# Kernel optimization log

Hardware: AMD Instinct MI355X
Metric: run time of the kernel (lower is better)

## Reference

```python
import jax, jax.numpy as jnp
import numpy as np

B, S_IMG, S_TXT, D, H, HD = 1, 2048, 512, 3072, 24, 128
A_TOK, A_DIM = 4, 1024
S_TOT = S_IMG + S_TXT
EPS = 1e-6
SCALE = 1.0


def _heads(x):
    # [B, S, D] -> [B, H, S, HD]
    return x.reshape(B, -1, H, HD).transpose(0, 2, 1, 3)


def _rms(x, w):
    return x * jax.lax.rsqrt(jnp.mean(x * x, axis=-1, keepdims=True) + EPS) * w


def _rope(x, cos, sin):
    # diffusers apply_rotary_emb, use_real=True, use_real_unbind_dim=-1
    xr = x.reshape(*x.shape[:-1], HD // 2, 2)
    x1, x2 = xr[..., 0], xr[..., 1]
    x_rot = jnp.stack([-x2, x1], axis=-1).reshape(x.shape)
    return x * cos + x_rot * sin


def _sdpa(q, k, v):
    scores = jnp.einsum('bhqd,bhkd->bhqk', q, k) / np.sqrt(HD).astype(np.float32)
    return jnp.einsum('bhqk,bhkd->bhqd', jax.nn.softmax(scores, axis=-1), v)


def setup_inputs() -> dict:
    key = jax.random.key(0)
    ks = jax.random.split(key, 24)
    s = 0.02
    inp = {
        'hidden_states': jax.random.normal(ks[0], (B, S_IMG, D), jnp.float32),
        'encoder_hidden_states': jax.random.normal(ks[1], (B, S_TXT, D), jnp.float32),
        'adapter_embeds': jax.random.normal(ks[2], (B, A_TOK, A_DIM), jnp.float32),
        'freqs_cos': jnp.cos(jax.random.normal(ks[3], (S_TOT, HD), jnp.float32)),
        'freqs_sin': jnp.sin(jax.random.normal(ks[3], (S_TOT, HD), jnp.float32)),
        'Wq': jax.random.normal(ks[4], (D, D), jnp.float32) * s,
        'bq': jnp.zeros((D,), jnp.float32),
        'Wk': jax.random.normal(ks[5], (D, D), jnp.float32) * s,
        'bk': jnp.zeros((D,), jnp.float32),
        'Wv': jax.random.normal(ks[6], (D, D), jnp.float32) * s,
        'bv': jnp.zeros((D,), jnp.float32),
        'norm_q_w': jnp.ones((HD,), jnp.float32),
        'norm_k_w': jnp.ones((HD,), jnp.float32),
        'Wq_add': jax.random.normal(ks[7], (D, D), jnp.float32) * s,
        'bq_add': jnp.zeros((D,), jnp.float32),
        'Wk_add': jax.random.normal(ks[8], (D, D), jnp.float32) * s,
        'bk_add': jnp.zeros((D,), jnp.float32),
        'Wv_add': jax.random.normal(ks[9], (D, D), jnp.float32) * s,
        'bv_add': jnp.zeros((D,), jnp.float32),
        'norm_added_q_w': jnp.ones((HD,), jnp.float32),
        'norm_added_k_w': jnp.ones((HD,), jnp.float32),
        'Wo': jax.random.normal(ks[10], (D, D), jnp.float32) * s,
        'bo': jnp.zeros((D,), jnp.float32),
        'Wo_add': jax.random.normal(ks[11], (D, D), jnp.float32) * s,
        'bo_add': jnp.zeros((D,), jnp.float32),
        'Wk_adapt': jax.random.normal(ks[12], (A_DIM, D), jnp.float32) * s,
        'Wv_adapt': jax.random.normal(ks[13], (A_DIM, D), jnp.float32) * s,
        'block_scaler': jnp.ones((1,), jnp.float32),
    }
    return inp


def reference(hidden_states, encoder_hidden_states, adapter_embeds, freqs_cos, freqs_sin,
              Wq, bq, Wk, bk, Wv, bv, norm_q_w, norm_k_w,
              Wq_add, bq_add, Wk_add, bk_add, Wv_add, bv_add,
              norm_added_q_w, norm_added_k_w, Wo, bo, Wo_add, bo_add,
              Wk_adapt, Wv_adapt, block_scaler):
    # image-token Q/K/V + per-head RMSNorm
    q = _rms(_heads(hidden_states @ Wq + bq), norm_q_w)
    k = _rms(_heads(hidden_states @ Wk + bk), norm_k_w)
    v = _heads(hidden_states @ Wv + bv)
    # text-token Q/K/V + per-head RMSNorm
    eq = _rms(_heads(encoder_hidden_states @ Wq_add + bq_add), norm_added_q_w)
    ek = _rms(_heads(encoder_hidden_states @ Wk_add + bk_add), norm_added_k_w)
    ev = _heads(encoder_hidden_states @ Wv_add + bv_add)
    # joint sequence: [text, image]
    q = jnp.concatenate([eq, q], axis=2)
    k = jnp.concatenate([ek, k], axis=2)
    v = jnp.concatenate([ev, v], axis=2)
    # RoPE on full joint sequence
    q = _rope(q, freqs_cos, freqs_sin)
    k = _rope(k, freqs_cos, freqs_sin)
    # main joint attention
    hs = _sdpa(q, k, v)                                    # [B,H,S_TOT,HD]
    hs = hs.transpose(0, 2, 1, 3).reshape(B, S_TOT, D)
    # adapter cross-attention (vision-direct branch)
    vd_k = _heads(adapter_embeds @ Wk_adapt)               # [B,H,A_TOK,HD]
    vd_v = _heads(adapter_embeds @ Wv_adapt)
    vd = _sdpa(q, vd_k, vd_v)
    vd = vd.transpose(0, 2, 1, 3).reshape(B, S_TOT, D)
    hs = hs + SCALE * (vd * block_scaler)
    # split back and project
    enc_out = hs[:, :S_TXT] @ Wo_add + bo_add
    img_out = hs[:, S_TXT:] @ Wo + bo
    return img_out, enc_out
```

## Files before the change

kernel.cpp:

```cpp
#include <hip/hip_runtime.h>

typedef unsigned short u16;
typedef short s16x8 __attribute__((ext_vector_type(8)));
typedef float f32x4 __attribute__((ext_vector_type(4)));

#define S_TXTC 512
#define S_TOTC 2560
#define DM 3072
#define NH 24
#define HDM 128

__device__ __forceinline__ float b2f(u16 u){ unsigned int i = ((unsigned int)u)<<16; float f; __builtin_memcpy(&f,&i,4); return f; }
__device__ __forceinline__ u16 f2b(float f){ unsigned int i; __builtin_memcpy(&i,&f,4); unsigned int r = i + 0x7FFFu + ((i>>16)&1u); return (u16)(r>>16); }
__device__ __forceinline__ s16x8 pk8(float4 a, float4 b){
  s16x8 r;
  r[0]=(short)f2b(a.x); r[1]=(short)f2b(a.y); r[2]=(short)f2b(a.z); r[3]=(short)f2b(a.w);
  r[4]=(short)f2b(b.x); r[5]=(short)f2b(b.y); r[6]=(short)f2b(b.z); r[7]=(short)f2b(b.w);
  return r;
}
__device__ __forceinline__ void g2l16(const void* g, void* l){
  __builtin_amdgcn_global_load_lds((const __attribute__((address_space(1))) void*)g,
                                   (__attribute__((address_space(3))) void*)l, 16, 0, 0);
}

__global__ __launch_bounds__(256) void fillv(float* __restrict__ p, int n, float v){
  int i = blockIdx.x*256 + threadIdx.x;
  if (i < n) p[i] = v;
}

__global__ __launch_bounds__(256) void cast_bf(const float* __restrict__ src, u16* __restrict__ dst, int n8){
  int i = blockIdx.x*256 + threadIdx.x;
  if (i < n8){
    float4 a = *(const float4*)(src + (size_t)i*8);
    float4 b = *(const float4*)(src + (size_t)i*8 + 4);
    *(s16x8*)(dst + (size_t)i*8) = pk8(a,b);
  }
}

__global__ __launch_bounds__(256) void catbias(const float* __restrict__ b0, const float* __restrict__ b1,
                                               const float* __restrict__ b2, float* __restrict__ dst){
  int i = blockIdx.x*256 + threadIdx.x;
  if (i < 9216) dst[i] = (i<3072)? b0[i] : (i<6144? b1[i-3072] : b2[i-6144]);
}

__global__ __launch_bounds__(256) void ktrans(const float* __restrict__ W, u16* __restrict__ Wt){
  __shared__ __align__(16) u16 t[64*72];
  int nt = blockIdx.x*64, kt_ = blockIdx.y*64;
  int tid = threadIdx.x;
  #pragma unroll
  for (int i=0;i<2;i++){
    int q = tid + 256*i;
    int r = q>>3, c8 = (q&7)*8;
    float4 f0 = *(const float4*)(W + (size_t)(kt_+r)*DM + nt + c8);
    float4 f1 = *(const float4*)(W + (size_t)(kt_+r)*DM + nt + c8 + 4);
    *(s16x8*)&t[r*72 + c8] = pk8(f0,f1);
  }
  __syncthreads();
  #pragma unroll
  for (int i=0;i<2;i++){
    int q = tid + 256*i;
    int n = q>>3, k8 = (q&7)*8;
    s16x8 v;
    #pragma unroll
    for (int j=0;j<8;j++) v[j] = (short)t[(k8+j)*72 + n];
    *(s16x8*)(Wt + (size_t)(nt+n)*DM + kt_ + k8) = v;
  }
}

template<int OUT32>
__device__ __forceinline__ void gcore(u16* la, u16* lb,
    const u16* __restrict__ A, const u16* __restrict__ Bt,
    const float* __restrict__ bias, void* __restrict__ Cv,
    int ldc, int rb, int crb, int cb){
  const int K = DM;
  int tid = threadIdx.x, w = tid>>6, l = tid&63, g = l>>4, c16 = l&15;
  int wr = (w>>1)*64, wc = (w&1)*64;
  f32x4 acc[4][4] = {};
  const u16* aL = A  + (size_t)(rb + w*32 + (l>>2))*K + (l&3)*8;
  const u16* bL = Bt + (size_t)(cb + w*32 + (l>>2))*K + (l&3)*8;
  u16* laB = la + w*1024;
  u16* lbB = lb + w*1024;
  for (int ks=0; ks<K; ks+=32){
    g2l16(aL + ks,              laB);
    g2l16(aL + 16*(size_t)K + ks, laB + 512);
    g2l16(bL + ks,              lbB);
    g2l16(bL + 16*(size_t)K + ks, lbB + 512);
    __syncthreads();
    s16x8 af[4], bf[4];
    #pragma unroll
    for (int m=0;m<4;m++) af[m] = *(const s16x8*)&la[(wr + m*16 + c16)*32 + g*8];
    #pragma unroll
    for (int n=0;n<4;n++) bf[n] = *(const s16x8*)&lb[(wc + n*16 + c16)*32 + g*8];
    #pragma unroll
    for (int m=0;m<4;m++)
      #pragma unroll
      for (int n=0;n<4;n++)
        acc[m][n] = __builtin_amdgcn_mfma_f32_16x16x32_bf16(af[m], bf[n], acc[m][n], 0,0,0);
    __syncthreads();
  }
  #pragma unroll
  for (int n=0;n<4;n++){
    int col = cb + wc + n*16 + c16;
    float bv = bias[col];
    #pragma unroll
    for (int m=0;m<4;m++){
      int r0 = crb + wr + m*16 + g*4;
      #pragma unroll
      for (int r=0;r<4;r++){
        float oo = acc[m][n][r] + bv;
        if (OUT32) ((float*)Cv)[(size_t)(r0+r)*ldc + col] = oo;
        else       ((u16*)Cv)[(size_t)(r0+r)*ldc + col] = f2b(oo);
      }
    }
  }
}

__global__ __launch_bounds__(256) void qkv_gemm(const u16* __restrict__ A, const u16* __restrict__ Bt,
                                                const float* __restrict__ bias, u16* __restrict__ C){
  __shared__ __align__(16) u16 la[4096];
  __shared__ __align__(16) u16 lb[4096];
  gcore<0>(la, lb, A, Bt, bias, C, 3*DM, blockIdx.x*128, blockIdx.x*128, blockIdx.y*128);
}

__global__ __launch_bounds__(256) void out_gemm(const u16* __restrict__ hsb,
    const u16* __restrict__ woT, const u16* __restrict__ woaT,
    const float* __restrict__ bo, const float* __restrict__ boa, float* __restrict__ out){
  __shared__ __align__(16) u16 la[4096];
  __shared__ __align__(16) u16 lb[4096];
  int bx = blockIdx.x;
  bool txt = (bx < 4);
  int rb = bx*128;
  const u16* Bt = txt? woaT : woT;
  const float* bias = txt? boa : bo;
  float* dst = txt? out + (size_t)2048*DM : out;
  int crb = txt? rb : rb - 512;
  gcore<1>(la, lb, hsb, Bt, bias, dst, DM, rb, crb, blockIdx.y*128);
}

__global__ __launch_bounds__(256) void epi_qk(
    const u16* __restrict__ qkvI, const u16* __restrict__ qkvT,
    const float* __restrict__ nqw, const float* __restrict__ nkw,
    const float* __restrict__ naq, const float* __restrict__ nak,
    const float* __restrict__ fcos, const float* __restrict__ fsin,
    u16* __restrict__ qh, u16* __restrict__ kh){
  int wid = blockIdx.x*4 + (threadIdx.x>>6);
  int lane = threadIdx.x&63;
  int which = wid / (NH*S_TOTC);
  int rem = wid % (NH*S_TOTC);
  int h = rem / S_TOTC, tok = rem % S_TOTC;
  const u16* src = ((tok<S_TXTC)? qkvT + (size_t)tok*(3*DM) : qkvI + (size_t)(tok-S_TXTC)*(3*DM))
                   + which*DM + h*HDM;
  const float* nw = which? ((tok<S_TXTC)? nak : nkw) : ((tok<S_TXTC)? naq : nqw);
  int d = lane*2;
  unsigned int u = *(const unsigned int*)(src + d);
  float x0 = b2f((u16)(u&0xffffu)), x1 = b2f((u16)(u>>16));
  float ss = x0*x0 + x1*x1;
  #pragma unroll
  for (int m=1;m<64;m<<=1) ss += __shfl_xor(ss, m);
  float rr = rsqrtf(ss*(1.f/128.f) + 1e-6f);
  float y0 = x0*rr*nw[d];
  float y1 = x1*rr*nw[d+1];
  float2 cc = *(const float2*)(fcos + (size_t)tok*HDM + d);
  float2 sn = *(const float2*)(fsin + (size_t)tok*HDM + d);
  float o0 = y0*cc.x - y1*sn.x;
  float o1 = y1*cc.y + y0*sn.y;
  u16* dst = (which? kh : qh) + ((size_t)h*S_TOTC + tok)*HDM + d;
  *(unsigned int*)dst = (unsigned int)f2b(o0) | ((unsigned int)f2b(o1)<<16);
}

__global__ __launch_bounds__(256) void epi_v(const u16* __restrict__ qkvI, const u16* __restrict__ qkvT,
                                             u16* __restrict__ vt){
  __shared__ __align__(16) u16 t[64*136];
  int h = blockIdx.x % NH, tb = blockIdx.x / NH;
  int tok0 = tb*64, tid = threadIdx.x;
  #pragma unroll
  for (int i=0;i<4;i++){
    int q = tid + 256*i;
    int tr = q>>4, c8 = (q&15)*8;
    int tok = tok0 + tr;
    const u16* src = ((tok<S_TXTC)? qkvT + (size_t)tok*(3*DM) : qkvI + (size_t)(tok-S_TXTC)*(3*DM))
                     + 2*DM + h*HDM;
    *(s16x8*)&t[tr*136 + c8] = *(const s16x8*)(src + c8);
  }
  __syncthreads();
  #pragma unroll
  for (int i=0;i<4;i++){
    int q = tid + 256*i;
    int d = q>>3, j8 = (q&7)*8;
    s16x8 v;
    #pragma unroll
    for (int j=0;j<8;j++) v[j] = (short)t[(j8+j)*136 + d];
    *(s16x8*)(vt + ((size_t)h*HDM + d)*S_TOTC + tok0 + j8) = v;
  }
}

__global__ __launch_bounds__(256) void adapterk(const float* __restrict__ ad, const float* __restrict__ Wk,
        const float* __restrict__ Wv, u16* __restrict__ vdk, u16* __restrict__ vdv){
  int wid = blockIdx.x*4 + (threadIdx.x>>6);
  int lane = threadIdx.x&63;
  int tensor = wid / (4*DM);
  int rem = wid % (4*DM);
  int tok = rem / DM, col = rem % DM;
  const float* Wp = tensor? Wv : Wk;
  float s = 0.f;
  #pragma unroll
  for (int i=0;i<16;i++){
    int k = lane + 64*i;
    s += ad[tok*1024 + k] * Wp[(size_t)k*DM + col];
  }
  #pragma unroll
  for (int m=1;m<64;m<<=1) s += __shfl_xor(s, m);
  if (lane==0){
    int hh = col>>7, d = col&127;
    (tensor? vdv : vdk)[(hh*4+tok)*HDM + d] = f2b(s);
  }
}

__global__ __launch_bounds__(256) void attnk(const u16* __restrict__ qh, const u16* __restrict__ kh,
    const u16* __restrict__ vt, const u16* __restrict__ vdk, const u16* __restrict__ vdv,
    const float* __restrict__ bscale, u16* __restrict__ hs){
  __shared__ __align__(16) u16 kts[64*136];
  __shared__ __align__(16) u16 vts[128*72];
  __shared__ __align__(16) u16 pwb[64*72];
  __shared__ __align__(16) u16 kad[16*136];
  __shared__ __align__(16) u16 vad[128*40];
  int h = blockIdx.y, qb = blockIdx.x*64;
  int tid = threadIdx.x, w = tid>>6, l = tid&63, g = l>>4, c16 = l&15;
  for (int e=tid; e<2048; e+=256){ int key=e>>7, d=e&127; kad[key*136+d] = (key<4)? vdk[(h*4+key)*HDM+d] : (u16)0; }
  for (int e=tid; e<4096; e+=256){ int d=e>>5, key=e&31; vad[d*40+key]   = (key<4)? vdv[(h*4+key)*HDM+d] : (u16)0; }
  int qrow = qb + w*16 + c16;
  s16x8 qf[4];
  #pragma unroll
  for (int kc=0;kc<4;kc++) qf[kc] = *(const s16x8*)(qh + ((size_t)h*S_TOTC + qrow)*HDM + kc*32 + g*8);
  f32x4 acc[8];
  #pragma unroll
  for (int dt=0;dt<8;dt++) acc[dt] = f32x4{0.f,0.f,0.f,0.f};
  float m_[4] = {-3e38f,-3e38f,-3e38f,-3e38f};
  float l_[4] = {0.f,0.f,0.f,0.f};
  const float scl = 0.08838834764831845f;
  const u16* khB = kh + (size_t)h*S_TOTC*HDM;
  const u16* vtB = vt + (size_t)h*HDM*S_TOTC;

  auto LOADT = [&](s16x8* kr, s16x8* vr, int kb){
    #pragma unroll
    for (int i=0;i<4;i++){
      int idx = tid + 256*i;
      kr[i] = *(const s16x8*)(khB + (size_t)(kb + (idx>>4))*HDM + (idx&15)*8);
      vr[i] = *(const s16x8*)(vtB + (size_t)(idx>>3)*S_TOTC + kb + (idx&7)*8);
    }
  };
  auto STORET = [&](s16x8* kr, s16x8* vr){
    #pragma unroll
    for (int i=0;i<4;i++){
      int idx = tid + 256*i;
      *(s16x8*)&kts[(idx>>4)*136 + (idx&15)*8] = kr[i];
      *(s16x8*)&vts[(idx>>3)*72 + (idx&7)*8] = vr[i];
    }
  };
  auto COMPUTE = [&](){
    f32x4 s[4];
    #pragma unroll
    for (int su=0;su<4;su++) s[su] = f32x4{0.f,0.f,0.f,0.f};
    __builtin_amdgcn_s_setprio(1);
    #pragma unroll
    for (int su=0;su<4;su++)
      #pragma unroll
      for (int kc=0;kc<4;kc++){
        s16x8 kf = *(const s16x8*)&kts[(su*16+c16)*136 + (kc*4+g)*8];
        s[su] = __builtin_amdgcn_mfma_f32_16x16x32_bf16(qf[kc], kf, s[su], 0,0,0);
      }
    __builtin_amdgcn_s_setprio(0);
    float tm[4], corr[4], rs[4];
    #pragma unroll
    for (int r=0;r<4;r++){
      #pragma unroll
      for (int su=0;su<4;su++) s[su][r] *= scl;
      tm[r] = fmaxf(fmaxf(s[0][r],s[1][r]), fmaxf(s[2][r],s[3][r]));
    }
    #pragma unroll
    for (int m=1;m<16;m<<=1)
      #pragma unroll
      for (int r=0;r<4;r++) tm[r] = fmaxf(tm[r], __shfl_xor(tm[r], m));
    #pragma unroll
    for (int r=0;r<4;r++){
      float mn = fmaxf(m_[r], tm[r]);
      corr[r] = __expf(m_[r]-mn);
      m_[r] = mn;
      rs[r] = 0.f;
      #pragma unroll
      for (int su=0;su<4;su++){ s[su][r] = __expf(s[su][r]-mn); rs[r] += s[su][r]; }
    }
    #pragma unroll
    for (int m=1;m<16;m<<=1)
      #pragma unroll
      for (int r=0;r<4;r++) rs[r] += __shfl_xor(rs[r], m);
    #pragma unroll
    for (int r=0;r<4;r++) l_[r] = l_[r]*corr[r] + rs[r];
    #pragma unroll
    for (int dt=0;dt<8;dt++)
      #pragma unroll
      for (int r=0;r<4;r++) acc[dt][r] *= corr[r];
    #pragma unroll
    for (int su=0;su<4;su++)
      #pragma unroll
      for (int r=0;r<4;r++)
        pwb[(w*16 + g*4 + r)*72 + su*16 + c16] = f2b(s[su][r]);
    s16x8 pf0 = *(const s16x8*)&pwb[(w*16 + c16)*72 + g*8];
    s16x8 pf1 = *(const s16x8*)&pwb[(w*16 + c16)*72 + 32 + g*8];
    __builtin_amdgcn_s_setprio(1);
    #pragma unroll
    for (int dt=0;dt<8;dt++){
      s16x8 vf0 = *(const s16x8*)&vts[(dt*16 + c16)*72 + g*8];
      acc[dt] = __builtin_amdgcn_mfma_f32_16x16x32_bf16(pf0, vf0, acc[dt], 0,0,0);
      s16x8 vf1 = *(const s16x8*)&vts[(dt*16 + c16)*72 + 32 + g*8];
      acc[dt] = __builtin_amdgcn_mfma_f32_16x16x32_bf16(pf1, vf1, acc[dt], 0,0,0);
    }
    __builtin_amdgcn_s_setprio(0);
  };

  s16x8 ka[4], va[4], kb2[4], vb2[4];
  LOADT(ka, va, 0);
  for (int kb=0; kb<S_TOTC; kb+=128){
    STORET(ka, va);
    __syncthreads();
    LOADT(kb2, vb2, kb+64);
    COMPUTE();
    __syncthreads();
    STORET(kb2, vb2);
    __syncthreads();
    if (kb+128 < S_TOTC) LOADT(ka, va, kb+128);
    COMPUTE();
    __syncthreads();
  }

  f32x4 s2 = {0.f,0.f,0.f,0.f};
  #pragma unroll
  for (int kc=0;kc<4;kc++){
    s16x8 kf = *(const s16x8*)&kad[c16*136 + (kc*4+g)*8];
    s2 = __builtin_amdgcn_mfma_f32_16x16x32_bf16(qf[kc], kf, s2, 0,0,0);
  }
  bool valid = (c16 < 4);
  float m2[4], l2[4];
  #pragma unroll
  for (int r=0;r<4;r++){ s2[r]*=scl; m2[r] = valid? s2[r] : -3e38f; }
  #pragma unroll
  for (int m=1;m<16;m<<=1)
    #pragma unroll
    for (int r=0;r<4;r++) m2[r] = fmaxf(m2[r], __shfl_xor(m2[r], m));
  #pragma unroll
  for (int r=0;r<4;r++){ float p = valid? __expf(s2[r]-m2[r]) : 0.f; s2[r]=p; l2[r]=p; }
  #pragma unroll
  for (int m=1;m<16;m<<=1)
    #pragma unroll
    for (int r=0;r<4;r++) l2[r] += __shfl_xor(l2[r], m);
  #pragma unroll
  for (int r=0;r<4;r++){
    pwb[(w*16 + g*4 + r)*72 + c16]      = f2b(s2[r]);
    pwb[(w*16 + g*4 + r)*72 + 16 + c16] = (u16)0;
  }
  s16x8 pf2 = *(const s16x8*)&pwb[(w*16 + c16)*72 + g*8];
  f32x4 a2[8];
  #pragma unroll
  for (int dt=0;dt<8;dt++) a2[dt] = f32x4{0.f,0.f,0.f,0.f};
  #pragma unroll
  for (int dt=0;dt<8;dt++){
    s16x8 vf = *(const s16x8*)&vad[(dt*16 + c16)*40 + g*8];
    a2[dt] = __builtin_amdgcn_mfma_f32_16x16x32_bf16(pf2, vf, a2[dt], 0,0,0);
  }
  float sb = bscale[0];
  #pragma unroll
  for (int dt=0;dt<8;dt++)
    #pragma unroll
    for (int r=0;r<4;r++){
      int tok = qb + w*16 + g*4 + r;
      int col = h*HDM + dt*16 + c16;
      hs[(size_t)tok*DM + col] = f2b(acc[dt][r]/l_[r] + sb*(a2[dt][r]/l2[r]));
    }
}

extern "C" void kernel_launch(void* const* d_in, const int* in_sizes, int n_in,
                              void* d_out, int out_size, void* d_ws, size_t ws_size,
                              hipStream_t stream){
  static const int expect[28] = {
    6291456, 1572864, 4096, 327680, 327680,
    9437184, 3072, 9437184, 3072, 9437184, 3072, 128, 128,
    9437184, 3072, 9437184, 3072, 9437184, 3072, 128, 128,
    9437184, 3072, 9437184, 3072, 3145728, 3145728, 1 };
  bool ok = (n_in == 28);
  if (ok) for (int i=0;i<28;i++) if (in_sizes[i] != expect[i]) { ok = false; break; }
  if (!ok){ fillv<<<(out_size+255)/256,256,0,stream>>>((float*)d_out, out_size, 7.0f); return; }
  if (ws_size < 119611392ull){ fillv<<<(out_size+255)/256,256,0,stream>>>((float*)d_out, out_size, 9.0f); return; }

  const float* hidden = (const float*)d_in[0];
  const float* enc    = (const float*)d_in[1];
  const float* adapt  = (const float*)d_in[2];
  const float* fcos   = (const float*)d_in[3];
  const float* fsin   = (const float*)d_in[4];
  const float* Wq  = (const float*)d_in[5];  const float* bq  = (const float*)d_in[6];
  const float* Wk  = (const float*)d_in[7];  const float* bk  = (const float*)d_in[8];
  const float* Wv  = (const float*)d_in[9];  const float* bv  = (const float*)d_in[10];
  const float* nqw = (const float*)d_in[11]; const float* nkw = (const float*)d_in[12];
  const float* Wqa = (const float*)d_in[13]; const float* bqa = (const float*)d_in[14];
  const float* Wka = (const float*)d_in[15]; const float* bka = (const float*)d_in[16];
  const float* Wva = (const float*)d_in[17]; const float* bva = (const float*)d_in[18];
  const float* naq = (const float*)d_in[19]; const float* nak = (const float*)d_in[20];
  const float* Wo  = (const float*)d_in[21]; const float* bo  = (const float*)d_in[22];
  const float* Woa = (const float*)d_in[23]; const float* boa = (const float*)d_in[24];
  const float* Wkad = (const float*)d_in[25]; const float* Wvad = (const float*)d_in[26];
  const float* bsc  = (const float*)d_in[27];
  float* out = (float*)d_out;

  char* ws = (char*)d_ws;
  u16* wt3   = (u16*)(ws);
  u16* kh    = (u16*)(ws);
  u16* vth   = (u16*)(ws + 15728640);
  u16* vdk   = (u16*)(ws + 31457280);
  u16* vdv   = (u16*)(ws + 31481856);
  u16* woaT  = (u16*)(ws + 33554432);
  u16* hbf   = (u16*)(ws + 56623104);
  u16* ebf   = (u16*)(ws + 69206016);
  u16* qh    = (u16*)(ws + 56623104);
  u16* qkvI  = (u16*)(ws + 72351744);
  u16* hsb   = (u16*)(ws + 72351744);
  u16* woT   = (u16*)(ws + 88080384);
  u16* qkvT  = (u16*)(ws + 110100480);
  float* biasA = (float*)(ws + 119537664);
  float* biasB = (float*)(ws + 119574528);

  dim3 tg(48,48);
  cast_bf<<<3072,256,0,stream>>>(hidden, hbf, 786432);
  cast_bf<<<768,256,0,stream>>>(enc, ebf, 196608);
  catbias<<<36,256,0,stream>>>(bq, bk, bv, biasA);
  catbias<<<36,256,0,stream>>>(bqa, bka, bva, biasB);
  ktrans<<<tg,256,0,stream>>>(Wq, wt3);
  ktrans<<<tg,256,0,stream>>>(Wk, wt3 + (size_t)DM*DM);
  ktrans<<<tg,256,0,stream>>>(Wv, wt3 + (size_t)2*DM*DM);
  qkv_gemm<<<dim3(16,72),256,0,stream>>>(hbf, wt3, biasA, qkvI);
  ktrans<<<tg,256,0,stream>>>(Wqa, wt3);
  ktrans<<<tg,256,0,stream>>>(Wka, wt3 + (size_t)DM*DM);
  ktrans<<<tg,256,0,stream>>>(Wva, wt3 + (size_t)2*DM*DM);
  qkv_gemm<<<dim3(4,72),256,0,stream>>>(ebf, wt3, biasB, qkvT);
  epi_qk<<<30720,256,0,stream>>>(qkvI, qkvT, nqw,nkw,naq,nak, fcos,fsin, qh, kh);
  epi_v<<<24*40,256,0,stream>>>(qkvI, qkvT, vth);
  adapterk<<<6144,256,0,stream>>>(adapt, Wkad, Wvad, vdk, vdv);
  attnk<<<dim3(40,24),256,0,stream>>>(qh, kh, vth, vdk, vdv, bsc, hsb);
  ktrans<<<tg,256,0,stream>>>(Wo, woT);
  ktrans<<<tg,256,0,stream>>>(Woa, woaT);
  out_gemm<<<dim3(20,24),256,0,stream>>>(hsb, woT, woaT, bo, boa, out);
}
```

Before: 780.7 us.

## Merge prep launches, fold softmax scale into Q, lazily rescale online softmax

Several independent changes ship together. The hidden/encoder casts, the two bias concatenations and groups of weight transposes are each merged into single launches. The 1/sqrt(d) softmax scale moves into the Q RoPE epilogue. The attention loop skips the accumulator rescale unless some row max grows by more than a threshold (8), and the final normalisation multiplies by reciprocals instead of dividing. The adapter K/V staging reuses the existing K/V LDS tiles, which lowers shared-memory use but leaves stale padding that relies on masking and zero probabilities.

```diff
diff --git a/kernel.cpp b/kernel.cpp
--- a/kernel.cpp
+++ b/kernel.cpp
@@ -28,22 +28,30 @@
   if (i < n) p[i] = v;
 }
 
-__global__ __launch_bounds__(256) void cast_bf(const float* __restrict__ src, u16* __restrict__ dst, int n8){
+__global__ __launch_bounds__(256) void cast2(const float* __restrict__ a, const float* __restrict__ b,
+                                             u16* __restrict__ dst, int na8, int n8){
   int i = blockIdx.x*256 + threadIdx.x;
-  if (i < n8){
-    float4 a = *(const float4*)(src + (size_t)i*8);
-    float4 b = *(const float4*)(src + (size_t)i*8 + 4);
-    *(s16x8*)(dst + (size_t)i*8) = pk8(a,b);
-  }
-}
-
-__global__ __launch_bounds__(256) void catbias(const float* __restrict__ b0, const float* __restrict__ b1,
-                                               const float* __restrict__ b2, float* __restrict__ dst){
+  if (i >= n8) return;
+  const float* src = (i < na8)? a + (size_t)i*8 : b + (size_t)(i-na8)*8;
+  float4 f0 = *(const float4*)src;
+  float4 f1 = *(const float4*)(src+4);
+  *(s16x8*)(dst + (size_t)i*8) = pk8(f0,f1);
+}
+
+__global__ __launch_bounds__(256) void catbias2(const float* __restrict__ b0, const float* __restrict__ b1,
+    const float* __restrict__ b2, const float* __restrict__ c0, const float* __restrict__ c1,
+    const float* __restrict__ c2, float* __restrict__ dst){
   int i = blockIdx.x*256 + threadIdx.x;
-  if (i < 9216) dst[i] = (i<3072)? b0[i] : (i<6144? b1[i-3072] : b2[i-6144]);
-}
-
-__global__ __launch_bounds__(256) void ktrans(const float* __restrict__ W, u16* __restrict__ Wt){
+  if (i >= 18432) return;
+  int j = (i < 9216)? i : i - 9216;
+  const float* s0 = (i<9216)? b0 : c0; const float* s1 = (i<9216)? b1 : c1; const float* s2 = (i<9216)? b2 : c2;
+  dst[i] = (j<3072)? s0[j] : (j<6144? s1[j-3072] : s2[j-6144]);
+}
+
+__global__ __launch_bounds__(256) void ktrans3(const float* __restrict__ W0, const float* __restrict__ W1,
+    const float* __restrict__ W2, u16* __restrict__ D0, u16* __restrict__ D1, u16* __restrict__ D2){
+  const float* W = (blockIdx.z==0)? W0 : ((blockIdx.z==1)? W1 : W2);
+  u16* Wt = (blockIdx.z==0)? D0 : ((blockIdx.z==1)? D1 : D2);
   __shared__ __align__(16) u16 t[64*72];
   int nt = blockIdx.x*64, kt_ = blockIdx.y*64;
   int tid = threadIdx.x;
@@ -81,9 +89,9 @@
   u16* laB = la + w*1024;
   u16* lbB = lb + w*1024;
   for (int ks=0; ks<K; ks+=32){
-    g2l16(aL + ks,              laB);
+    g2l16(aL + ks,                laB);
     g2l16(aL + 16*(size_t)K + ks, laB + 512);
-    g2l16(bL + ks,              lbB);
+    g2l16(bL + ks,                lbB);
     g2l16(bL + 16*(size_t)K + ks, lbB + 512);
     __syncthreads();
     s16x8 af[4], bf[4];
@@ -162,8 +170,9 @@
   float y1 = x1*rr*nw[d+1];
   float2 cc = *(const float2*)(fcos + (size_t)tok*HDM + d);
   float2 sn = *(const float2*)(fsin + (size_t)tok*HDM + d);
-  float o0 = y0*cc.x - y1*sn.x;
-  float o1 = y1*cc.y + y0*sn.y;
+  float sc = which? 1.0f : 0.08838834764831845f;
+  float o0 = (y0*cc.x - y1*sn.x)*sc;
+  float o1 = (y1*cc.y + y0*sn.y)*sc;
   u16* dst = (which? kh : qh) + ((size_t)h*S_TOTC + tok)*HDM + d;
   *(unsigned int*)dst = (unsigned int)f2b(o0) | ((unsigned int)f2b(o1)<<16);
 }
@@ -222,12 +231,8 @@
   __shared__ __align__(16) u16 kts[64*136];
   __shared__ __align__(16) u16 vts[128*72];
   __shared__ __align__(16) u16 pwb[64*72];
-  __shared__ __align__(16) u16 kad[16*136];
-  __shared__ __align__(16) u16 vad[128*40];
   int h = blockIdx.y, qb = blockIdx.x*64;
   int tid = threadIdx.x, w = tid>>6, l = tid&63, g = l>>4, c16 = l&15;
-  for (int e=tid; e<2048; e+=256){ int key=e>>7, d=e&127; kad[key*136+d] = (key<4)? vdk[(h*4+key)*HDM+d] : (u16)0; }
-  for (int e=tid; e<4096; e+=256){ int d=e>>5, key=e&31; vad[d*40+key]   = (key<4)? vdv[(h*4+key)*HDM+d] : (u16)0; }
   int qrow = qb + w*16 + c16;
   s16x8 qf[4];
   #pragma unroll
@@ -237,7 +242,6 @@
   for (int dt=0;dt<8;dt++) acc[dt] = f32x4{0.f,0.f,0.f,0.f};
   float m_[4] = {-3e38f,-3e38f,-3e38f,-3e38f};
   float l_[4] = {0.f,0.f,0.f,0.f};
-  const float scl = 0.08838834764831845f;
   const u16* khB = kh + (size_t)h*S_TOTC*HDM;
   const u16* vtB = vt + (size_t)h*HDM*S_TOTC;
 
@@ -270,36 +274,42 @@
         s[su] = __builtin_amdgcn_mfma_f32_16x16x32_bf16(qf[kc], kf, s[su], 0,0,0);
       }
     __builtin_amdgcn_s_setprio(0);
-    float tm[4], corr[4], rs[4];
+    float tm[4];
+    #pragma unroll
+    for (int r=0;r<4;r++)
+      tm[r] = fmaxf(fmaxf(s[0][r],s[1][r]), fmaxf(s[2][r],s[3][r]));
+    #pragma unroll
+    for (int m=1;m<16;m<<=1)
+      #pragma unroll
+      for (int r=0;r<4;r++) tm[r] = fmaxf(tm[r], __shfl_xor(tm[r], m));
+    bool need = !__all(tm[0]<=m_[0]+8.f && tm[1]<=m_[1]+8.f && tm[2]<=m_[2]+8.f && tm[3]<=m_[3]+8.f);
+    if (need){
+      float corr[4];
+      #pragma unroll
+      for (int r=0;r<4;r++){
+        float mn = fmaxf(m_[r], tm[r]);
+        corr[r] = __expf(m_[r]-mn);
+        m_[r] = mn;
+        l_[r] *= corr[r];
+      }
+      #pragma unroll
+      for (int dt=0;dt<8;dt++)
+        #pragma unroll
+        for (int r=0;r<4;r++) acc[dt][r] *= corr[r];
+    }
+    float rs[4];
     #pragma unroll
     for (int r=0;r<4;r++){
-      #pragma unroll
-      for (int su=0;su<4;su++) s[su][r] *= scl;
-      tm[r] = fmaxf(fmaxf(s[0][r],s[1][r]), fmaxf(s[2][r],s[3][r]));
+      rs[r] = 0.f;
+      #pragma unroll
+      for (int su=0;su<4;su++){ s[su][r] = __expf(s[su][r]-m_[r]); rs[r] += s[su][r]; }
     }
     #pragma unroll
     for (int m=1;m<16;m<<=1)
       #pragma unroll
-      for (int r=0;r<4;r++) tm[r] = fmaxf(tm[r], __shfl_xor(tm[r], m));
-    #pragma unroll
-    for (int r=0;r<4;r++){
-      float mn = fmaxf(m_[r], tm[r]);
-      corr[r] = __expf(m_[r]-mn);
-      m_[r] = mn;
-      rs[r] = 0.f;
-      #pragma unroll
-      for (int su=0;su<4;su++){ s[su][r] = __expf(s[su][r]-mn); rs[r] += s[su][r]; }
-    }
-    #pragma unroll
-    for (int m=1;m<16;m<<=1)
-      #pragma unroll
       for (int r=0;r<4;r++) rs[r] += __shfl_xor(rs[r], m);
     #pragma unroll
-    for (int r=0;r<4;r++) l_[r] = l_[r]*corr[r] + rs[r];
-    #pragma unroll
-    for (int dt=0;dt<8;dt++)
-      #pragma unroll
-      for (int r=0;r<4;r++) acc[dt][r] *= corr[r];
+    for (int r=0;r<4;r++) l_[r] += rs[r];
     #pragma unroll
     for (int su=0;su<4;su++)
       #pragma unroll
@@ -333,16 +343,25 @@
     __syncthreads();
   }
 
+  if (tid < 64){
+    int key = tid>>4, c8 = (tid&15)*8;
+    *(s16x8*)&kts[key*136 + c8] = *(const s16x8*)(vdk + (h*4+key)*HDM + c8);
+  } else if (tid < 192){
+    int d = tid - 64;
+    #pragma unroll
+    for (int key=0;key<4;key++) vts[d*72 + key] = vdv[(h*4+key)*HDM + d];
+  }
+  __syncthreads();
   f32x4 s2 = {0.f,0.f,0.f,0.f};
   #pragma unroll
   for (int kc=0;kc<4;kc++){
-    s16x8 kf = *(const s16x8*)&kad[c16*136 + (kc*4+g)*8];
+    s16x8 kf = *(const s16x8*)&kts[c16*136 + (kc*4+g)*8];
     s2 = __builtin_amdgcn_mfma_f32_16x16x32_bf16(qf[kc], kf, s2, 0,0,0);
   }
   bool valid = (c16 < 4);
   float m2[4], l2[4];
   #pragma unroll
-  for (int r=0;r<4;r++){ s2[r]*=scl; m2[r] = valid? s2[r] : -3e38f; }
+  for (int r=0;r<4;r++) m2[r] = valid? s2[r] : -3e38f;
   #pragma unroll
   for (int m=1;m<16;m<<=1)
     #pragma unroll
@@ -364,17 +383,20 @@
   for (int dt=0;dt<8;dt++) a2[dt] = f32x4{0.f,0.f,0.f,0.f};
   #pragma unroll
   for (int dt=0;dt<8;dt++){
-    s16x8 vf = *(const s16x8*)&vad[(dt*16 + c16)*40 + g*8];
+    s16x8 vf = *(const s16x8*)&vts[(dt*16 + c16)*72 + g*8];
     a2[dt] = __builtin_amdgcn_mfma_f32_16x16x32_bf16(pf2, vf, a2[dt], 0,0,0);
   }
   float sb = bscale[0];
+  float rl[4], rl2[4];
+  #pragma unroll
+  for (int r=0;r<4;r++){ rl[r] = 1.f/l_[r]; rl2[r] = sb/l2[r]; }
   #pragma unroll
   for (int dt=0;dt<8;dt++)
     #pragma unroll
     for (int r=0;r<4;r++){
       int tok = qb + w*16 + g*4 + r;
       int col = h*HDM + dt*16 + c16;
-      hs[(size_t)tok*DM + col] = f2b(acc[dt][r]/l_[r] + sb*(a2[dt][r]/l2[r]));
+      hs[(size_t)tok*DM + col] = f2b(acc[dt][r]*rl[r] + a2[dt][r]*rl2[r]);
     }
 }
 
@@ -428,23 +450,16 @@
   float* biasB = (float*)(ws + 119574528);
 
   dim3 tg(48,48);
-  cast_bf<<<3072,256,0,stream>>>(hidden, hbf, 786432);
-  cast_bf<<<768,256,0,stream>>>(enc, ebf, 196608);
-  catbias<<<36,256,0,stream>>>(bq, bk, bv, biasA);
-  catbias<<<36,256,0,stream>>>(bqa, bka, bva, biasB);
-  ktrans<<<tg,256,0,stream>>>(Wq, wt3);
-  ktrans<<<tg,256,0,stream>>>(Wk, wt3 + (size_t)DM*DM);
-  ktrans<<<tg,256,0,stream>>>(Wv, wt3 + (size_t)2*DM*DM);
+  cast2<<<3840,256,0,stream>>>(hidden, enc, hbf, 786432, 983040);
+  catbias2<<<72,256,0,stream>>>(bq,bk,bv, bqa,bka,bva, biasA);
+  ktrans3<<<dim3(48,48,3),256,0,stream>>>(Wq, Wk, Wv, wt3, wt3 + (size_t)DM*DM, wt3 + (size_t)2*DM*DM);
   qkv_gemm<<<dim3(16,72),256,0,stream>>>(hbf, wt3, biasA, qkvI);
-  ktrans<<<tg,256,0,stream>>>(Wqa, wt3);
-  ktrans<<<tg,256,0,stream>>>(Wka, wt3 + (size_t)DM*DM);
-  ktrans<<<tg,256,0,stream>>>(Wva, wt3 + (size_t)2*DM*DM);
+  ktrans3<<<dim3(48,48,3),256,0,stream>>>(Wqa, Wka, Wva, wt3, wt3 + (size_t)DM*DM, wt3 + (size_t)2*DM*DM);
   qkv_gemm<<<dim3(4,72),256,0,stream>>>(ebf, wt3, biasB, qkvT);
   epi_qk<<<30720,256,0,stream>>>(qkvI, qkvT, nqw,nkw,naq,nak, fcos,fsin, qh, kh);
   epi_v<<<24*40,256,0,stream>>>(qkvI, qkvT, vth);
   adapterk<<<6144,256,0,stream>>>(adapt, Wkad, Wvad, vdk, vdv);
   attnk<<<dim3(40,24),256,0,stream>>>(qh, kh, vth, vdk, vdv, bsc, hsb);
-  ktrans<<<tg,256,0,stream>>>(Wo, woT);
-  ktrans<<<tg,256,0,stream>>>(Woa, woaT);
+  ktrans3<<<dim3(48,48,2),256,0,stream>>>(Wo, Woa, Woa, woT, woaT, woaT);
   out_gemm<<<dim3(20,24),256,0,stream>>>(hsb, woT, woaT, bo, boa, out);
 }
```

Measured after the change: 747.8 us. 1.04x faster.
